# Performance work log

Measured on AMD Instinct MI355X. Metric: run time of the kernel, lower is better.

## Reference

```python
import jax, jax.numpy as jnp
import numpy as np

B, S, E = 2, 4096, 768
NH, D = 12, 64
W = 256            # one-sided attention window (attention_window=512 // 2)
NEG = jnp.float32(-1e30)  # stands in for -inf at invalid band positions (safe grads)


def setup_inputs() -> dict:
    key = jax.random.key(0)
    ks = jax.random.split(key, 4)
    sc = 0.02
    return {
        'hidden_states': jax.random.normal(ks[0], (B, S, E), jnp.float32),
        'attention_mask': jnp.zeros((B, S), jnp.float32),   # 0 = local attention everywhere
        'is_index_masked': jnp.zeros((B, S), bool),
        'Wq': jax.random.normal(ks[1], (E, E), jnp.float32) * sc,
        'bq': jnp.zeros((E,), jnp.float32),
        'Wk': jax.random.normal(ks[2], (E, E), jnp.float32) * sc,
        'bk': jnp.zeros((E,), jnp.float32),
        'Wv': jax.random.normal(ks[3], (E, E), jnp.float32) * sc,
        'bv': jnp.zeros((E,), jnp.float32),
    }


def _longformer_local(hidden_states, attention_mask, is_index_masked, Wq, bq, Wk, bk, Wv, bv):
    b, s, e = hidden_states.shape
    w = W
    nc = s // w
    # projections (nn.Linear: x @ W.T + b); query pre-scaled by 1/sqrt(head_dim)
    q = (hidden_states @ Wq.T + bq) / jnp.sqrt(jnp.float32(D))
    k = hidden_states @ Wk.T + bk
    v = hidden_states @ Wv.T + bv
    # [B, NH, S, D]
    q = q.reshape(b, s, NH, D).transpose(0, 2, 1, 3)
    k = k.reshape(b, s, NH, D).transpose(0, 2, 1, 3)
    v = v.reshape(b, s, NH, D).transpose(0, 2, 1, 3)

    # pad keys/values by w on each side; chunk into [B,NH,nc,3w,D] windows
    kp = jnp.pad(k, ((0, 0), (0, 0), (w, w), (0, 0)))
    vp = jnp.pad(v, ((0, 0), (0, 0), (w, w), (0, 0)))
    starts = jnp.arange(nc) * w                      # [nc]
    cidx = starts[:, None] + jnp.arange(3 * w)[None, :]  # [nc, 3w] (padded coords)
    kc = kp[:, :, cidx, :]                            # [B,NH,nc,3w,D]
    vc = vp[:, :, cidx, :]                            # [B,NH,nc,3w,D]
    qc = q.reshape(b, NH, nc, w, D)

    # banded scores: query p in chunk attends keys at offsets p..p+2w within the 3w window
    scores = jnp.einsum('bhcpd,bhckd->bhcpk', qc, kc)  # [B,NH,nc,w,3w]
    p = jnp.arange(w)[:, None]
    koff = jnp.arange(2 * w + 1)[None, :]
    band_idx = p + koff                                # [w, 2w+1]
    band = jnp.take_along_axis(scores, band_idx[None, None, None], axis=-1)  # [B,NH,nc,w,2w+1]

    # additive mask from attention_mask (torch: finfo.min where !=0), gathered at key positions
    fmask = jnp.where(attention_mask != 0, jnp.finfo(jnp.float32).min, jnp.float32(0.0))  # [B,S]
    j = starts[:, None, None] + band_idx[None] - w     # global key index [nc,w,2w+1]
    valid = (j >= 0) & (j < s)
    jc = jnp.clip(j, 0, s - 1)
    band = band + fmask[:, jc][:, None]                # [B,1->NH,nc,w,2w+1]
    # _mask_invalid_locations: out-of-sequence band entries -> -inf (NEG)
    band = jnp.where(valid[None, None], band, NEG)

    probs = jax.nn.softmax(band.astype(jnp.float32), axis=-1)
    # zero probs at fully-masked query positions
    im = is_index_masked.reshape(b, 1, nc, w, 1)
    probs = jnp.where(im, jnp.float32(0.0), probs)

    # scatter band back to [B,NH,nc,w,3w] and contract with value chunks
    full = jnp.zeros((b, NH, nc, w, 3 * w), probs.dtype).at[:, :, :, p, band_idx].set(probs)
    out = jnp.einsum('bhcpk,bhckd->bhcpd', full, vc)   # [B,NH,nc,w,D]
    out = out.reshape(b, NH, s, D).transpose(0, 2, 1, 3).reshape(b, s, e)
    return out


def reference(hidden_states, attention_mask, is_index_masked, Wq, bq, Wk, bk, Wv, bv):
    return _longformer_local(hidden_states, attention_mask, is_index_masked,
                             Wq, bq, Wk, bk, Wv, bv)
```

## Files before the change

### kernel.cpp

```cpp
#include <hip/hip_runtime.h>

typedef __bf16 bf16;
typedef __attribute__((ext_vector_type(8))) __bf16 bf16x8;
typedef __attribute__((ext_vector_type(4))) __bf16 bf16x4;
typedef __attribute__((ext_vector_type(4))) float f32x4;

#define MFMA16(a, b, c) __builtin_amdgcn_mfma_f32_16x16x32_bf16((a), (b), (c), 0, 0, 0)

#define S_LEN 4096
#define NHEAD 12
#define EMB   768
#define NEGV  (-1e30f)

__device__ __forceinline__ void gload16(const bf16* g, bf16* l) {
  __builtin_amdgcn_global_load_lds((const __attribute__((address_space(1))) void*)g,
                                   (__attribute__((address_space(3))) void*)l, 16, 0, 0);
}

__global__ __launch_bounds__(256) void cvt_kernel(const float* __restrict__ x,
                                                  bf16* __restrict__ o, int n8, float scale) {
  int i = blockIdx.x * 256 + threadIdx.x;
  if (i >= n8) return;
  const float4* p = (const float4*)(x + (size_t)i * 8);
  float4 a = p[0], b = p[1];
  bf16x8 v;
  v[0] = (bf16)(a.x * scale); v[1] = (bf16)(a.y * scale);
  v[2] = (bf16)(a.z * scale); v[3] = (bf16)(a.w * scale);
  v[4] = (bf16)(b.x * scale); v[5] = (bf16)(b.y * scale);
  v[6] = (bf16)(b.z * scale); v[7] = (bf16)(b.w * scale);
  *(bf16x8*)(o + (size_t)i * 8) = v;
}

__global__ __launch_bounds__(256) void cvt3_kernel(const float* __restrict__ w0,
                                                   const float* __restrict__ w1,
                                                   const float* __restrict__ w2,
                                                   bf16* __restrict__ o, int n8) {
  int which = blockIdx.y;
  const float* src = (which == 0) ? w0 : (which == 1) ? w1 : w2;
  float scale = (which == 0) ? 0.125f : 1.0f;
  int i = blockIdx.x * 256 + threadIdx.x;
  if (i >= n8) return;
  const float4* p = (const float4*)(src + (size_t)i * 8);
  float4 a = p[0], b = p[1];
  bf16x8 v;
  v[0] = (bf16)(a.x * scale); v[1] = (bf16)(a.y * scale);
  v[2] = (bf16)(a.z * scale); v[3] = (bf16)(a.w * scale);
  v[4] = (bf16)(b.x * scale); v[5] = (bf16)(b.y * scale);
  v[6] = (bf16)(b.z * scale); v[7] = (bf16)(b.w * scale);
  *(bf16x8*)(o + ((size_t)which * n8 + i) * 8) = v;
}

__global__ __launch_bounds__(256) void qkv_gemm(const bf16* __restrict__ Xb, const bf16* __restrict__ Wb,
                                                const float* __restrict__ bq, const float* __restrict__ bk,
                                                const float* __restrict__ bv,
                                                bf16* __restrict__ Qo, bf16* __restrict__ Ko,
                                                bf16* __restrict__ Vt) {
  __shared__ union SM {
    struct { bf16 a[2][128 * 64]; bf16 b2[2][128 * 64]; } st;
    bf16 c[128 * 130];
  } sm;
  const int tid = threadIdx.x;
  const int l = tid & 63, w = tid >> 6;
  const int ln = l & 15, g = l >> 4;
  const int wm = w >> 1, wn = w & 1;
  const int m0 = blockIdx.x * 128;
  const int n0 = blockIdx.y * 128;

  const f32x4 zero4 = {0.f, 0.f, 0.f, 0.f};
  f32x4 acc[4][4];
#pragma unroll
  for (int i = 0; i < 4; ++i)
#pragma unroll
    for (int j = 0; j < 4; ++j) acc[i][j] = zero4;

  int srow[4], sslot[4];
#pragma unroll
  for (int i = 0; i < 4; ++i) {
    const int G = w * 256 + i * 64 + l;
    srow[i] = G >> 3;
    sslot[i] = (G & 7) ^ (srow[i] & 7);
  }

  auto stage = [&](int sb, int kt) {
    const int k0 = kt * 64;
#pragma unroll
    for (int i = 0; i < 4; ++i) {
      gload16(Xb + (size_t)(m0 + srow[i]) * 768 + k0 + sslot[i] * 8, &sm.st.a[sb][(w * 256 + i * 64) * 8]);
      gload16(Wb + (size_t)(n0 + srow[i]) * 768 + k0 + sslot[i] * 8, &sm.st.b2[sb][(w * 256 + i * 64) * 8]);
    }
  };

  stage(0, 0);
  __syncthreads();

  int buf = 0;
  for (int kt = 0; kt < 12; ++kt, buf ^= 1) {
    if (kt < 11) stage(buf ^ 1, kt + 1);
#pragma unroll
    for (int kc = 0; kc < 2; ++kc) {
      bf16x8 af[4], bfr[4];
#pragma unroll
      for (int i = 0; i < 4; ++i) {
        int ra = wm * 64 + i * 16 + ln;
        af[i] = *(const bf16x8*)(&sm.st.a[buf][ra * 64 + ((kc * 4 + g) ^ (ra & 7)) * 8]);
        int rb = wn * 64 + i * 16 + ln;
        bfr[i] = *(const bf16x8*)(&sm.st.b2[buf][rb * 64 + ((kc * 4 + g) ^ (rb & 7)) * 8]);
      }
#pragma unroll
      for (int mi = 0; mi < 4; ++mi)
#pragma unroll
        for (int ni = 0; ni < 4; ++ni)
          acc[mi][ni] = MFMA16(af[mi], bfr[ni], acc[mi][ni]);
    }
    __syncthreads();
  }

  const int which = n0 / 768;
  const int h0 = (n0 % 768) >> 6;
  const int b = m0 >> 12;
  const int h = h0 + wn;
  const float bsc = (which == 0) ? 0.125f : 1.0f;
  const float* bias = (which == 0) ? bq : (which == 1) ? bk : bv;
  float bvv[4];
#pragma unroll
  for (int ni = 0; ni < 4; ++ni) bvv[ni] = bias[h * 64 + ni * 16 + ln] * bsc;

#pragma unroll
  for (int mi = 0; mi < 4; ++mi)
#pragma unroll
    for (int ni = 0; ni < 4; ++ni)
#pragma unroll
      for (int r = 0; r < 4; ++r) {
        int sl = wm * 64 + mi * 16 + g * 4 + r;
        sm.c[sl * 130 + wn * 64 + ni * 16 + ln] = (bf16)(acc[mi][ni][r] + bvv[ni]);
      }
  __syncthreads();

  if (which < 2) {
    bf16* dst = (which == 0) ? Qo : Ko;
#pragma unroll
    for (int it = 0; it < 8; ++it) {
      int gid = it * 256 + tid;
      int sl = gid >> 4, cg = gid & 15;
      int hh = h0 + (cg >> 3);
      bf16x8 v8 = *(const bf16x8*)(&sm.c[sl * 130 + cg * 8]);
      *(bf16x8*)(dst + ((size_t)(b * NHEAD + hh) * S_LEN + (m0 & 4095) + sl) * 64 + (cg & 7) * 8) = v8;
    }
  } else {
#pragma unroll
    for (int it = 0; it < 4; ++it) {
      int d = it * 32 + (tid >> 3);
      int scp = tid & 7;
      int hh = h0 + (d >> 6);
      bf16x8 o0, o1;
#pragma unroll
      for (int i2 = 0; i2 < 8; ++i2) o0[i2] = sm.c[(scp * 16 + i2) * 130 + d];
#pragma unroll
      for (int i2 = 0; i2 < 8; ++i2) o1[i2] = sm.c[(scp * 16 + 8 + i2) * 130 + d];
      bf16* dp = Vt + ((size_t)(b * NHEAD + hh) * 64 + (d & 63)) * S_LEN + (m0 & 4095) + scp * 16;
      *(bf16x8*)dp = o0;
      *(bf16x8*)(dp + 8) = o1;
    }
  }
}

__global__ __launch_bounds__(512) void attn_kernel(const bf16* __restrict__ Qb, const bf16* __restrict__ Kb,
                                                   const bf16* __restrict__ Vtb,
                                                   const float* __restrict__ amask,
                                                   const unsigned char* __restrict__ imask,
                                                   float* __restrict__ out) {
  __shared__ bf16 Ks[2][64 * 64];
  __shared__ bf16 Vs[2][64 * 64];
  __shared__ bf16 Pt[8][16 * 64];
  __shared__ float Ams[2][64];
  const int tid = threadIdx.x;
  const int l = tid & 63, w = tid >> 6;
  const int ln = l & 15, g = l >> 4;
  const int orig = blockIdx.x;
  const int lb = (orig & 7) * 96 + (orig >> 3);
  const int qc = lb & 31, bh = lb >> 5;
  const int b = bh / NHEAD, h = bh % NHEAD;
  const int q0 = qc * 128;
  const int qg = q0 + w * 16 + ln;

  const size_t qoff = ((size_t)bh * S_LEN + qg) * 64;
  const bf16x8 qf0 = *(const bf16x8*)(Qb + qoff + g * 8);
  const bf16x8 qf1 = *(const bf16x8*)(Qb + qoff + 32 + g * 8);

  const f32x4 zero4 = {0.f, 0.f, 0.f, 0.f};
  f32x4 acc[4];
#pragma unroll
  for (int i = 0; i < 4; ++i) acc[i] = zero4;
  float mrun = -1e38f, lrun = 0.f;

  const int t_lo = (q0 >= 256) ? 0 : ((256 - q0) >> 6);
  int t_hi = (S_LEN + 256 - q0) >> 6;
  if (t_hi > 10) t_hi = 10;

  auto stage = [&](int sb, int t) {
    const int tj0 = q0 - 256 + t * 64;
    const int G = w * 64 + l;
    const int row = G >> 3, dsl = G & 7;
    const int slot = dsl ^ (row & 7);
    gload16(Kb + ((size_t)bh * S_LEN + tj0 + row) * 64 + slot * 8, &Ks[sb][w * 512]);
    gload16(Vtb + ((size_t)bh * 64 + row) * S_LEN + tj0 + slot * 8, &Vs[sb][w * 512]);
    if (tid < 64) {
      float am = amask[b * S_LEN + tj0 + tid];
      Ams[sb][tid] = (am != 0.f) ? -1e30f : 0.f;
    }
  };

  stage(0, t_lo);
  asm volatile("s_waitcnt vmcnt(0)" ::: "memory");
  __syncthreads();

  int buf = 0;
  for (int t = t_lo; t < t_hi; ++t, buf ^= 1) {
    if (t + 1 < t_hi) stage(buf ^ 1, t + 1);
    const int tj0 = q0 - 256 + t * 64;

    f32x4 sc[4];
#pragma unroll
    for (int i = 0; i < 4; ++i) sc[i] = zero4;
    __builtin_amdgcn_s_setprio(1);
#pragma unroll
    for (int kc = 0; kc < 2; ++kc) {
      bf16x8 qf = kc ? qf1 : qf0;
#pragma unroll
      for (int mi = 0; mi < 4; ++mi) {
        int r = mi * 16 + ln;
        bf16x8 kf = *(const bf16x8*)(&Ks[buf][r * 64 + ((kc * 4 + g) ^ (r & 7)) * 8]);
        sc[mi] = MFMA16(kf, qf, sc[mi]);
      }
    }
    __builtin_amdgcn_s_setprio(0);

    float mt = -1e38f;
    const bool full = (t * 64 >= w * 16 + 15) && (t * 64 <= w * 16 + 449);
    if (full) {
#pragma unroll
      for (int mi = 0; mi < 4; ++mi)
#pragma unroll
        for (int r = 0; r < 4; ++r) {
          int key = mi * 16 + g * 4 + r;
          float v = sc[mi][r] + Ams[buf][key];
          sc[mi][r] = v;
          mt = fmaxf(mt, v);
        }
    } else {
#pragma unroll
      for (int mi = 0; mi < 4; ++mi)
#pragma unroll
        for (int r = 0; r < 4; ++r) {
          int key = mi * 16 + g * 4 + r;
          int j = tj0 + key;
          bool valid = (j >= qg - 256) && (j <= qg + 256);
          float v = valid ? (sc[mi][r] + Ams[buf][key]) : NEGV;
          sc[mi][r] = v;
          mt = fmaxf(mt, v);
        }
    }
    mt = fmaxf(mt, __shfl_xor(mt, 16));
    mt = fmaxf(mt, __shfl_xor(mt, 32));
    if (!__all(mt <= mrun + 8.f)) {
      float mnew = fmaxf(mrun, mt);
      float corr = __expf(mrun - mnew);
      lrun *= corr;
#pragma unroll
      for (int i = 0; i < 4; ++i) acc[i] *= corr;
      mrun = mnew;
    }
    float psum = 0.f;
    float pv[4][4];
#pragma unroll
    for (int mi = 0; mi < 4; ++mi)
#pragma unroll
      for (int r = 0; r < 4; ++r) {
        float p = __expf(sc[mi][r] - mrun);
        pv[mi][r] = p;
        psum += p;
      }
    psum += __shfl_xor(psum, 16);
    psum += __shfl_xor(psum, 32);
    lrun += psum;

    bf16* PtW = &Pt[w][0];
#pragma unroll
    for (int mi = 0; mi < 4; ++mi) {
      bf16x4 pk;
      pk[0] = (bf16)pv[mi][0]; pk[1] = (bf16)pv[mi][1];
      pk[2] = (bf16)pv[mi][2]; pk[3] = (bf16)pv[mi][3];
      *(bf16x4*)(&PtW[ln * 64 + ((mi * 4 + g) ^ ln) * 4]) = pk;
    }

    __builtin_amdgcn_s_setprio(1);
#pragma unroll
    for (int ds2 = 0; ds2 < 4; ++ds2) {
#pragma unroll
      for (int kc = 0; kc < 2; ++kc) {
        int r = ds2 * 16 + ln;
        bf16x8 vf = *(const bf16x8*)(&Vs[buf][r * 64 + ((kc * 4 + g) ^ (r & 7)) * 8]);
        bf16x4 pa = *(const bf16x4*)(&PtW[ln * 64 + ((kc * 8 + g * 2) ^ ln) * 4]);
        bf16x4 pb = *(const bf16x4*)(&PtW[ln * 64 + ((kc * 8 + g * 2 + 1) ^ ln) * 4]);
        bf16x8 pf = __builtin_shufflevector(pa, pb, 0, 1, 2, 3, 4, 5, 6, 7);
        acc[ds2] = MFMA16(vf, pf, acc[ds2]);
      }
    }
    __builtin_amdgcn_s_setprio(0);

    asm volatile("s_waitcnt vmcnt(0)" ::: "memory");
    __syncthreads();
  }

  float rl = 1.0f / lrun;
  if (imask[b * S_LEN + qg] != 0) rl = 0.0f;
  float* ob = out + ((size_t)b * S_LEN + qg) * EMB + h * 64;
#pragma unroll
  for (int ds2 = 0; ds2 < 4; ++ds2) {
    float4 o;
    o.x = acc[ds2][0] * rl; o.y = acc[ds2][1] * rl;
    o.z = acc[ds2][2] * rl; o.w = acc[ds2][3] * rl;
    *(float4*)(ob + ds2 * 16 + g * 4) = o;
  }
}

extern "C" void kernel_launch(void* const* d_in, const int* in_sizes, int n_in,
                              void* d_out, int out_size, void* d_ws, size_t ws_size,
                              hipStream_t stream) {
  const float* X = (const float*)d_in[0];
  const float* amask = (const float*)d_in[1];
  const unsigned char* imask = (const unsigned char*)d_in[2];
  const float* Wq = (const float*)d_in[3];
  const float* bq = (const float*)d_in[4];
  const float* Wk = (const float*)d_in[5];
  const float* bk = (const float*)d_in[6];
  const float* Wv = (const float*)d_in[7];
  const float* bv = (const float*)d_in[8];
  float* out = (float*)d_out;

  bf16* Xb = (bf16*)d_ws;
  bf16* Wb = Xb + 6291456;
  bf16* Qb = Wb + 3 * 589824;
  bf16* Kb = Qb + 6291456;
  bf16* Vt = Kb + 6291456;

  cvt_kernel<<<3072, 256, 0, stream>>>(X, Xb, 6291456 / 8, 1.0f);
  cvt3_kernel<<<dim3(288, 3), 256, 0, stream>>>(Wq, Wk, Wv, Wb, 589824 / 8);
  qkv_gemm<<<dim3(64, 18), 256, 0, stream>>>(Xb, Wb, bq, bk, bv, Qb, Kb, Vt);
  attn_kernel<<<768, 512, 0, stream>>>(Qb, Kb, Vt, amask, imask, out);
}
```

Before: 172.2 us.

## Load K/V fragments directly from global into registers, dropping LDS staging

```diff
diff --git a/kernel.cpp b/kernel.cpp
--- a/kernel.cpp
+++ b/kernel.cpp
@@ -50,6 +50,12 @@
   *(bf16x8*)(o + ((size_t)which * n8 + i) * 8) = v;
 }
 
+__global__ __launch_bounds__(256) void amask_cvt(const float* __restrict__ am,
+                                                 float* __restrict__ o, int n) {
+  int i = blockIdx.x * 256 + threadIdx.x;
+  if (i < n) o[i] = (am[i] != 0.f) ? -1e30f : 0.f;
+}
+
 __global__ __launch_bounds__(256) void qkv_gemm(const bf16* __restrict__ Xb, const bf16* __restrict__ Wb,
                                                 const float* __restrict__ bq, const float* __restrict__ bk,
                                                 const float* __restrict__ bv,
@@ -164,29 +170,30 @@
   }
 }
 
-__global__ __launch_bounds__(512) void attn_kernel(const bf16* __restrict__ Qb, const bf16* __restrict__ Kb,
+__global__ __launch_bounds__(256) void attn_kernel(const bf16* __restrict__ Qb, const bf16* __restrict__ Kb,
                                                    const bf16* __restrict__ Vtb,
-                                                   const float* __restrict__ amask,
+                                                   const float* __restrict__ Amadd,
                                                    const unsigned char* __restrict__ imask,
                                                    float* __restrict__ out) {
-  __shared__ bf16 Ks[2][64 * 64];
-  __shared__ bf16 Vs[2][64 * 64];
-  __shared__ bf16 Pt[8][16 * 64];
-  __shared__ float Ams[2][64];
+  __shared__ bf16 Pt[4][16 * 64];
   const int tid = threadIdx.x;
   const int l = tid & 63, w = tid >> 6;
   const int ln = l & 15, g = l >> 4;
   const int orig = blockIdx.x;
-  const int lb = (orig & 7) * 96 + (orig >> 3);
-  const int qc = lb & 31, bh = lb >> 5;
+  const int lb = (orig & 7) * 192 + (orig >> 3);
+  const int qc = lb & 63, bh = lb >> 6;
   const int b = bh / NHEAD, h = bh % NHEAD;
-  const int q0 = qc * 128;
+  const int q0 = qc * 64;
   const int qg = q0 + w * 16 + ln;
 
   const size_t qoff = ((size_t)bh * S_LEN + qg) * 64;
   const bf16x8 qf0 = *(const bf16x8*)(Qb + qoff + g * 8);
   const bf16x8 qf1 = *(const bf16x8*)(Qb + qoff + 32 + g * 8);
 
+  const bf16* Kbh = Kb + (size_t)bh * S_LEN * 64;
+  const bf16* Vbh = Vtb + (size_t)bh * 64 * S_LEN;
+  const float* Ab = Amadd + b * S_LEN;
+
   const f32x4 zero4 = {0.f, 0.f, 0.f, 0.f};
   f32x4 acc[4];
 #pragma unroll
@@ -195,29 +202,28 @@
 
   const int t_lo = (q0 >= 256) ? 0 : ((256 - q0) >> 6);
   int t_hi = (S_LEN + 256 - q0) >> 6;
-  if (t_hi > 10) t_hi = 10;
-
-  auto stage = [&](int sb, int t) {
+  if (t_hi > 9) t_hi = 9;
+
+  bf16x8 kf[4][2];
+  {
+    const int tj0 = q0 - 256 + t_lo * 64;
+#pragma unroll
+    for (int mi = 0; mi < 4; ++mi)
+#pragma unroll
+      for (int kc = 0; kc < 2; ++kc)
+        kf[mi][kc] = *(const bf16x8*)(Kbh + (size_t)(tj0 + mi * 16 + ln) * 64 + kc * 32 + g * 8);
+  }
+
+  bf16* PtW = &Pt[w][0];
+  for (int t = t_lo; t < t_hi; ++t) {
     const int tj0 = q0 - 256 + t * 64;
-    const int G = w * 64 + l;
-    const int row = G >> 3, dsl = G & 7;
-    const int slot = dsl ^ (row & 7);
-    gload16(Kb + ((size_t)bh * S_LEN + tj0 + row) * 64 + slot * 8, &Ks[sb][w * 512]);
-    gload16(Vtb + ((size_t)bh * 64 + row) * S_LEN + tj0 + slot * 8, &Vs[sb][w * 512]);
-    if (tid < 64) {
-      float am = amask[b * S_LEN + tj0 + tid];
-      Ams[sb][tid] = (am != 0.f) ? -1e30f : 0.f;
-    }
-  };
-
-  stage(0, t_lo);
-  asm volatile("s_waitcnt vmcnt(0)" ::: "memory");
-  __syncthreads();
-
-  int buf = 0;
-  for (int t = t_lo; t < t_hi; ++t, buf ^= 1) {
-    if (t + 1 < t_hi) stage(buf ^ 1, t + 1);
-    const int tj0 = q0 - 256 + t * 64;
+
+    bf16x8 vf[4][2];
+#pragma unroll
+    for (int ds2 = 0; ds2 < 4; ++ds2)
+#pragma unroll
+      for (int kc = 0; kc < 2; ++kc)
+        vf[ds2][kc] = *(const bf16x8*)(Vbh + (size_t)(ds2 * 16 + ln) * S_LEN + tj0 + kc * 32 + g * 8);
 
     f32x4 sc[4];
 #pragma unroll
@@ -227,14 +233,22 @@
     for (int kc = 0; kc < 2; ++kc) {
       bf16x8 qf = kc ? qf1 : qf0;
 #pragma unroll
-      for (int mi = 0; mi < 4; ++mi) {
-        int r = mi * 16 + ln;
-        bf16x8 kf = *(const bf16x8*)(&Ks[buf][r * 64 + ((kc * 4 + g) ^ (r & 7)) * 8]);
-        sc[mi] = MFMA16(kf, qf, sc[mi]);
-      }
+      for (int mi = 0; mi < 4; ++mi) sc[mi] = MFMA16(kf[mi][kc], qf, sc[mi]);
     }
     __builtin_amdgcn_s_setprio(0);
 
+    if (t + 1 < t_hi) {
+      const int nj0 = tj0 + 64;
+#pragma unroll
+      for (int mi = 0; mi < 4; ++mi)
+#pragma unroll
+        for (int kc = 0; kc < 2; ++kc)
+          kf[mi][kc] = *(const bf16x8*)(Kbh + (size_t)(nj0 + mi * 16 + ln) * 64 + kc * 32 + g * 8);
+    }
+
+    f32x4 am[4];
+#pragma unroll
+    for (int mi = 0; mi < 4; ++mi) am[mi] = *(const f32x4*)(Ab + tj0 + mi * 16 + g * 4);
     float mt = -1e38f;
     const bool full = (t * 64 >= w * 16 + 15) && (t * 64 <= w * 16 + 449);
     if (full) {
@@ -242,8 +256,7 @@
       for (int mi = 0; mi < 4; ++mi)
 #pragma unroll
         for (int r = 0; r < 4; ++r) {
-          int key = mi * 16 + g * 4 + r;
-          float v = sc[mi][r] + Ams[buf][key];
+          float v = sc[mi][r] + am[mi][r];
           sc[mi][r] = v;
           mt = fmaxf(mt, v);
         }
@@ -252,10 +265,9 @@
       for (int mi = 0; mi < 4; ++mi)
 #pragma unroll
         for (int r = 0; r < 4; ++r) {
-          int key = mi * 16 + g * 4 + r;
-          int j = tj0 + key;
+          int j = tj0 + mi * 16 + g * 4 + r;
           bool valid = (j >= qg - 256) && (j <= qg + 256);
-          float v = valid ? (sc[mi][r] + Ams[buf][key]) : NEGV;
+          float v = valid ? (sc[mi][r] + am[mi][r]) : NEGV;
           sc[mi][r] = v;
           mt = fmaxf(mt, v);
         }
@@ -284,7 +296,6 @@
     psum += __shfl_xor(psum, 32);
     lrun += psum;
 
-    bf16* PtW = &Pt[w][0];
 #pragma unroll
     for (int mi = 0; mi < 4; ++mi) {
       bf16x4 pk;
@@ -298,18 +309,13 @@
     for (int ds2 = 0; ds2 < 4; ++ds2) {
 #pragma unroll
       for (int kc = 0; kc < 2; ++kc) {
-        int r = ds2 * 16 + ln;
-        bf16x8 vf = *(const bf16x8*)(&Vs[buf][r * 64 + ((kc * 4 + g) ^ (r & 7)) * 8]);
         bf16x4 pa = *(const bf16x4*)(&PtW[ln * 64 + ((kc * 8 + g * 2) ^ ln) * 4]);
         bf16x4 pb = *(const bf16x4*)(&PtW[ln * 64 + ((kc * 8 + g * 2 + 1) ^ ln) * 4]);
         bf16x8 pf = __builtin_shufflevector(pa, pb, 0, 1, 2, 3, 4, 5, 6, 7);
-        acc[ds2] = MFMA16(vf, pf, acc[ds2]);
+        acc[ds2] = MFMA16(vf[ds2][kc], pf, acc[ds2]);
       }
     }
     __builtin_amdgcn_s_setprio(0);
-
-    asm volatile("s_waitcnt vmcnt(0)" ::: "memory");
-    __syncthreads();
   }
 
   float rl = 1.0f / lrun;
@@ -343,9 +349,11 @@
   bf16* Qb = Wb + 3 * 589824;
   bf16* Kb = Qb + 6291456;
   bf16* Vt = Kb + 6291456;
+  float* Amadd = (float*)(Vt + 6291456);
 
   cvt_kernel<<<3072, 256, 0, stream>>>(X, Xb, 6291456 / 8, 1.0f);
   cvt3_kernel<<<dim3(288, 3), 256, 0, stream>>>(Wq, Wk, Wv, Wb, 589824 / 8);
+  amask_cvt<<<32, 256, 0, stream>>>(amask, Amadd, 2 * S_LEN);
   qkv_gemm<<<dim3(64, 18), 256, 0, stream>>>(Xb, Wb, bq, bk, bv, Qb, Kb, Vt);
-  attn_kernel<<<768, 512, 0, stream>>>(Qb, Kb, Vt, amask, imask, out);
-}
+  attn_kernel<<<1536, 256, 0, stream>>>(Qb, Kb, Vt, Amadd, imask, out);
+}
```

Result: slower. 246.0 us (+42.8%).
